# Performance work log

Hardware: AMD Instinct MI355X
Metric: run time of the kernel (lower is better)

## Reference

```python
import jax, jax.numpy as jnp
import numpy as np
import math

BS, N = 32, 2048
INPUT_SIZE, HIDDEN, NUM_LAYERS = 128, 64, 4
ALPHA, LAMDA = 0.1, 1.0
EPS = 1e-5
EDGE_P = 0.01


def setup_inputs() -> dict:
    key = jax.random.key(0)
    ks = jax.random.split(key, 6)
    x = jax.random.normal(ks[0], (BS, N, INPUT_SIZE), jnp.float32)
    adj = (jax.random.uniform(ks[1], (BS, N, N)) < EDGE_P).astype(jnp.float32)
    adj = adj * (1.0 - jnp.eye(N, dtype=jnp.float32))  # no pre-existing self loops
    proj_w = jax.random.normal(ks[2], (INPUT_SIZE, HIDDEN), jnp.float32) * (1.0 / math.sqrt(INPUT_SIZE))
    proj_b = jnp.zeros((HIDDEN,), jnp.float32)
    ln_g = jnp.ones((NUM_LAYERS, HIDDEN), jnp.float32)
    ln_b = jnp.zeros((NUM_LAYERS, HIDDEN), jnp.float32)
    conv_w = jax.random.normal(ks[3], (NUM_LAYERS, HIDDEN, HIDDEN), jnp.float32) * (1.0 / math.sqrt(HIDDEN))
    head_w = jax.random.normal(ks[4], (HIDDEN, 1), jnp.float32) * (1.0 / math.sqrt(HIDDEN))
    head_b = jnp.zeros((1,), jnp.float32)
    return dict(x=x, adj=adj, proj_w=proj_w, proj_b=proj_b, ln_g=ln_g, ln_b=ln_b,
                conv_w=conv_w, head_w=head_w, head_b=head_b)


def _layer_norm(h, g, b):
    mu = h.mean(-1, keepdims=True)
    var = ((h - mu) ** 2).mean(-1, keepdims=True)
    return (h - mu) * jax.lax.rsqrt(var + EPS) * g + b


def _gcn_norm(adj):
    # A_hat = D^{-1/2} (A + I) D^{-1/2}; only the nonzero pattern of adj is used,
    # matching adj.nonzero() -> edge_index with unit edge weights + added self loops.
    a = (adj != 0).astype(adj.dtype) + jnp.eye(adj.shape[-1], dtype=adj.dtype)
    dinv = jax.lax.rsqrt(a.sum(-1))  # deg >= 1 thanks to self loops
    return a * dinv[:, :, None] * dinv[:, None, :]


def _forward(x, adj_hat, proj_w, proj_b, ln_g, ln_b, conv_w, head_w, head_b):
    h = x @ proj_w + proj_b  # [bs, N, hidden]
    for i in range(NUM_LAYERS):
        beta = math.log(LAMDA / (i + 1) + 1.0)  # GCNII identity-mapping strength
        # DeepGCNLayer block='res+': h_in -> norm -> act -> conv, then residual add
        z = jax.nn.relu(_layer_norm(h, ln_g[i], ln_b[i]))
        p = jnp.einsum('bij,bjd->bid', adj_hat, z)          # neighbor aggregation
        s = (1.0 - ALPHA) * p + ALPHA * z                   # initial residual (x0 = conv input)
        h = h + (1.0 - beta) * s + beta * (s @ conv_w[i])   # GCN2Conv out + res+ skip
    return h @ head_w + head_b  # [bs, N, 1]


def reference(x, adj, proj_w, proj_b, ln_g, ln_b, conv_w, head_w, head_b):
    return _forward(x, _gcn_norm(adj), proj_w, proj_b, ln_g, ln_b, conv_w, head_w, head_b)
```

## Files before the change

### kernel.cpp

```cpp
#include <hip/hip_runtime.h>
#include <math.h>

#define BS 32
#define N 2048
#define ROWS (BS * N)
#define IN 128
#define HID 64
#define K_CAP 80
#define EPS 1e-5f
#define ALPHA 0.1f

typedef float fx4 __attribute__((ext_vector_type(4)));

__global__ __launch_bounds__(256) void k_build(const float* __restrict__ adj,
                                               int* __restrict__ ell,
                                               int* __restrict__ cnt,
                                               float* __restrict__ dinv) {
    int lane = threadIdx.x & 63;
    int row  = blockIdx.x * 4 + (threadIdx.x >> 6);
    const fx4* arow = (const fx4*)(adj + (size_t)row * N);
    int* erow = ell + (size_t)row * K_CAP;
    int base = 0;
#pragma unroll
    for (int it = 0; it < N / 256; it++) {
        fx4 f = __builtin_nontemporal_load(&arow[it * 64 + lane]);
#pragma unroll
        for (int k = 0; k < 4; k++) {
            float v = f[k];
            unsigned long long m = __ballot(v != 0.0f);
            if (v != 0.0f) {
                int pos = base + __popcll(m & ((1ull << lane) - 1ull));
                if (pos < K_CAP) erow[pos] = it * 256 + lane * 4 + k;
            }
            base += __popcll(m);
        }
    }
    if (lane == 0) {
        cnt[row]  = base < K_CAP ? base : K_CAP;
        dinv[row] = rsqrtf((float)base + 1.0f);
    }
}

__global__ __launch_bounds__(256) void k_proj_ln(const float* __restrict__ x,
                                                 const float* __restrict__ w,
                                                 const float* __restrict__ b,
                                                 const float* __restrict__ g0,
                                                 const float* __restrict__ b0,
                                                 float* __restrict__ h,
                                                 float* __restrict__ z0) {
    __shared__ float sw[IN * HID];
    __shared__ float sx[4][IN];
    int tx = threadIdx.x;
    for (int i = tx; i < IN * HID; i += 256) sw[i] = w[i];
    int row0 = blockIdx.x * 4;
    if (tx < 128) {
        float4 v = *(const float4*)(x + (size_t)(row0 + (tx >> 5)) * IN + (tx & 31) * 4);
        *(float4*)&sx[tx >> 5][(tx & 31) * 4] = v;
    }
    __syncthreads();
    int c = tx & 63, r = tx >> 6;
    float acc = b[c];
#pragma unroll
    for (int k = 0; k < IN; k += 4) {
        float4 xa = *(const float4*)&sx[r][k];
        acc += xa.x * sw[(k + 0) * HID + c];
        acc += xa.y * sw[(k + 1) * HID + c];
        acc += xa.z * sw[(k + 2) * HID + c];
        acc += xa.w * sw[(k + 3) * HID + c];
    }
    size_t idx = (size_t)(row0 + r) * HID + c;
    h[idx] = acc;
    float sum = acc;
    for (int o = 32; o >= 1; o >>= 1) sum += __shfl_xor(sum, o);
    float mu = sum * (1.0f / 64.0f);
    float d  = acc - mu;
    float vs = d * d;
    for (int o = 32; o >= 1; o >>= 1) vs += __shfl_xor(vs, o);
    float rr = rsqrtf(vs * (1.0f / 64.0f) + EPS);
    float zz = d * rr * g0[c] + b0[c];
    z0[idx] = zz > 0.0f ? zz : 0.0f;
}

__global__ __launch_bounds__(256) void k_layer(
    float* __restrict__ h, const float* __restrict__ z_in,
    float* __restrict__ z_out,
    const int* __restrict__ ell, const int* __restrict__ cnt,
    const float* __restrict__ dinv, const float* __restrict__ w,
    const float* __restrict__ g_next, const float* __restrict__ b_next,
    float beta, int is_last,
    const float* __restrict__ head_w, const float* __restrict__ head_b,
    float* __restrict__ out) {
    __shared__ float sw[HID * HID];
    __shared__ float ss[16][HID];
    int tx = threadIdx.x;
    int lane = tx & 63, wid = tx >> 6;
    int p = lane & 15, q = lane >> 4;

    int bid = blockIdx.x;
    int swz = (bid & 7) * (int)(gridDim.x >> 3) + (bid >> 3);
    int row0 = swz * 16 + wid * 4;
    int jbase = row0 & ~(N - 1);

    for (int i = tx; i < HID * HID; i += 256) sw[i] = w[i];

    int   nn[4];
    float di[4];
    int   myidx[4];
    float myw[4];
    float4 zi4[4];
#pragma unroll
    for (int rr = 0; rr < 4; rr++) {
        int row = row0 + rr;
        nn[rr] = cnt[row];
        di[rr] = dinv[row];
        zi4[rr] = *(const float4*)(z_in + (size_t)row * HID + 4 * p);
        myidx[rr] = 0; myw[rr] = 0.0f;
        if (lane < nn[rr]) {
            myidx[rr] = ell[(size_t)row * K_CAP + lane];
            myw[rr]   = dinv[jbase + myidx[rr]];
        }
    }

    float4 acc[4];
#pragma unroll
    for (int rr = 0; rr < 4; rr++) acc[rr] = make_float4(0.f, 0.f, 0.f, 0.f);
    int ntm = 0;
#pragma unroll
    for (int rr = 0; rr < 4; rr++) {
        int nm = nn[rr] < 64 ? nn[rr] : 64;
        nm = (nm + 3) & ~3;
        ntm = nm > ntm ? nm : ntm;
    }
    for (int t = q; t < ntm; t += 4) {
#pragma unroll
        for (int rr = 0; rr < 4; rr++) {
            int   j  = jbase + __shfl(myidx[rr], t);
            float wj = __shfl(myw[rr], t);
            float4 zj = *(const float4*)(z_in + (size_t)j * HID + 4 * p);
            acc[rr].x += wj * zj.x; acc[rr].y += wj * zj.y;
            acc[rr].z += wj * zj.z; acc[rr].w += wj * zj.w;
        }
    }
#pragma unroll
    for (int rr = 0; rr < 4; rr++) {
        for (int t = 64 + q; t < nn[rr]; t += 4) {
            int   j  = jbase + ell[(size_t)(row0 + rr) * K_CAP + t];
            float wj = dinv[j];
            float4 zj = *(const float4*)(z_in + (size_t)j * HID + 4 * p);
            acc[rr].x += wj * zj.x; acc[rr].y += wj * zj.y;
            acc[rr].z += wj * zj.z; acc[rr].w += wj * zj.w;
        }
    }
#pragma unroll
    for (int rr = 0; rr < 4; rr++) {
        float4 a = acc[rr];
        a.x += __shfl_xor(a.x, 16); a.y += __shfl_xor(a.y, 16);
        a.z += __shfl_xor(a.z, 16); a.w += __shfl_xor(a.w, 16);
        a.x += __shfl_xor(a.x, 32); a.y += __shfl_xor(a.y, 32);
        a.z += __shfl_xor(a.z, 32); a.w += __shfl_xor(a.w, 32);
        float dd = di[rr];
        float4 s4;
        s4.x = (1.0f - ALPHA) * dd * (a.x + dd * zi4[rr].x) + ALPHA * zi4[rr].x;
        s4.y = (1.0f - ALPHA) * dd * (a.y + dd * zi4[rr].y) + ALPHA * zi4[rr].y;
        s4.z = (1.0f - ALPHA) * dd * (a.z + dd * zi4[rr].z) + ALPHA * zi4[rr].z;
        s4.w = (1.0f - ALPHA) * dd * (a.w + dd * zi4[rr].w) + ALPHA * zi4[rr].w;
        if (q == 0) *(float4*)&ss[wid * 4 + rr][4 * p] = s4;
    }
    __syncthreads();

#pragma unroll
    for (int rr = 0; rr < 4; rr++) {
        int row = row0 + rr;
        float mv = 0.0f;
#pragma unroll
        for (int k = 0; k < HID; k += 4) {
            float4 sk = *(const float4*)&ss[wid * 4 + rr][k];
            mv += sk.x * sw[(k + 0) * HID + lane];
            mv += sk.y * sw[(k + 1) * HID + lane];
            mv += sk.z * sw[(k + 2) * HID + lane];
            mv += sk.w * sw[(k + 3) * HID + lane];
        }
        float s_c = ss[wid * 4 + rr][lane];
        size_t idx = (size_t)row * HID + lane;
        float hn = __builtin_nontemporal_load(h + idx) +
                   (1.0f - beta) * s_c + beta * mv;
        if (!is_last) {
            __builtin_nontemporal_store(hn, h + idx);
            float sum = hn;
            for (int o = 32; o >= 1; o >>= 1) sum += __shfl_xor(sum, o);
            float mu = sum * (1.0f / 64.0f);
            float d  = hn - mu;
            float vs = d * d;
            for (int o = 32; o >= 1; o >>= 1) vs += __shfl_xor(vs, o);
            float rv = rsqrtf(vs * (1.0f / 64.0f) + EPS);
            float zz = d * rv * g_next[lane] + b_next[lane];
            z_out[idx] = zz > 0.0f ? zz : 0.0f;
        } else {
            float v = hn * head_w[lane];
            for (int o = 32; o >= 1; o >>= 1) v += __shfl_xor(v, o);
            if (lane == 0) out[row] = v + head_b[0];
        }
    }
}

extern "C" void kernel_launch(void* const* d_in, const int* in_sizes, int n_in,
                              void* d_out, int out_size, void* d_ws, size_t ws_size,
                              hipStream_t stream) {
    const float* x      = (const float*)d_in[0];
    const float* adj    = (const float*)d_in[1];
    const float* proj_w = (const float*)d_in[2];
    const float* proj_b = (const float*)d_in[3];
    const float* ln_g   = (const float*)d_in[4];
    const float* ln_b   = (const float*)d_in[5];
    const float* conv_w = (const float*)d_in[6];
    const float* head_w = (const float*)d_in[7];
    const float* head_b = (const float*)d_in[8];
    float* out = (float*)d_out;

    float* h    = (float*)d_ws;
    float* za   = h + (size_t)ROWS * HID;
    float* zb   = za + (size_t)ROWS * HID;
    float* dinv = zb + (size_t)ROWS * HID;
    int*   cnt  = (int*)(dinv + ROWS);
    int*   ell  = cnt + ROWS;

    dim3 blk(256);

    k_build<<<dim3(ROWS / 4), blk, 0, stream>>>(adj, ell, cnt, dinv);
    k_proj_ln<<<dim3(ROWS / 4), blk, 0, stream>>>(x, proj_w, proj_b, ln_g, ln_b, h, za);

    float* zin = za;
    float* zout = zb;
    for (int i = 0; i < 4; i++) {
        float beta = (float)log(1.0 / (double)(i + 1) + 1.0);
        int last = (i == 3);
        int gi = (i + 1) < 3 ? (i + 1) : 3;
        k_layer<<<dim3(ROWS / 16), blk, 0, stream>>>(h, zin, zout, ell, cnt, dinv,
                                                     conv_w + (size_t)i * HID * HID,
                                                     ln_g + gi * HID, ln_b + gi * HID,
                                                     beta, last, head_w, head_b, out);
        float* t = zin; zin = zout; zout = t;
    }
}
```

Before: 407.0 us.

## Drop shared weight tile in layer kernel, read weights from global, raise occupancy

Removes the 16KB shared-memory copy of the conv weight and the block-wide barrier. The matvec now reads the weight directly from global/L1 and reuses each loaded weight across the wave's four rows. Also sets launch bounds to 8 waves per SIMD, defers the self-row z/dinv loads to lower register pressure, and uses 32-bit unsigned indexing with a precomputed batch base pointer. The intent is to cut LDS usage and register pressure so more blocks can be resident, which helps hide the latency of the gather. The cost is more global/L1 weight traffic and a risk of spilling under the tighter register bound. Dropping the barrier appears safe because each wave reads back only the ss rows it wrote itself.

```diff
diff --git a/kernel.cpp b/kernel.cpp
--- a/kernel.cpp
+++ b/kernel.cpp
@@ -81,7 +81,7 @@
     z0[idx] = zz > 0.0f ? zz : 0.0f;
 }
 
-__global__ __launch_bounds__(256) void k_layer(
+__global__ __launch_bounds__(256, 8) void k_layer(
     float* __restrict__ h, const float* __restrict__ z_in,
     float* __restrict__ z_out,
     const int* __restrict__ ell, const int* __restrict__ cnt,
@@ -90,7 +90,6 @@
     float beta, int is_last,
     const float* __restrict__ head_w, const float* __restrict__ head_b,
     float* __restrict__ out) {
-    __shared__ float sw[HID * HID];
     __shared__ float ss[16][HID];
     int tx = threadIdx.x;
     int lane = tx & 63, wid = tx >> 6;
@@ -100,30 +99,22 @@
     int swz = (bid & 7) * (int)(gridDim.x >> 3) + (bid >> 3);
     int row0 = swz * 16 + wid * 4;
     int jbase = row0 & ~(N - 1);
-
-    for (int i = tx; i < HID * HID; i += 256) sw[i] = w[i];
+    const float4* zb4 = (const float4*)z_in + (unsigned)jbase * 16u;
+    const float4* zr4 = (const float4*)z_in;
 
     int   nn[4];
-    float di[4];
     int   myidx[4];
     float myw[4];
-    float4 zi4[4];
 #pragma unroll
     for (int rr = 0; rr < 4; rr++) {
         int row = row0 + rr;
         nn[rr] = cnt[row];
-        di[rr] = dinv[row];
-        zi4[rr] = *(const float4*)(z_in + (size_t)row * HID + 4 * p);
         myidx[rr] = 0; myw[rr] = 0.0f;
         if (lane < nn[rr]) {
-            myidx[rr] = ell[(size_t)row * K_CAP + lane];
+            myidx[rr] = ell[(unsigned)row * K_CAP + lane];
             myw[rr]   = dinv[jbase + myidx[rr]];
         }
     }
-
-    float4 acc[4];
-#pragma unroll
-    for (int rr = 0; rr < 4; rr++) acc[rr] = make_float4(0.f, 0.f, 0.f, 0.f);
     int ntm = 0;
 #pragma unroll
     for (int rr = 0; rr < 4; rr++) {
@@ -131,12 +122,16 @@
         nm = (nm + 3) & ~3;
         ntm = nm > ntm ? nm : ntm;
     }
+
+    float4 acc[4];
+#pragma unroll
+    for (int rr = 0; rr < 4; rr++) acc[rr] = make_float4(0.f, 0.f, 0.f, 0.f);
     for (int t = q; t < ntm; t += 4) {
 #pragma unroll
         for (int rr = 0; rr < 4; rr++) {
-            int   j  = jbase + __shfl(myidx[rr], t);
+            int   j  = __shfl(myidx[rr], t);
             float wj = __shfl(myw[rr], t);
-            float4 zj = *(const float4*)(z_in + (size_t)j * HID + 4 * p);
+            float4 zj = zb4[(unsigned)(j * 16 + p)];
             acc[rr].x += wj * zj.x; acc[rr].y += wj * zj.y;
             acc[rr].z += wj * zj.z; acc[rr].w += wj * zj.w;
         }
@@ -144,13 +139,15 @@
 #pragma unroll
     for (int rr = 0; rr < 4; rr++) {
         for (int t = 64 + q; t < nn[rr]; t += 4) {
-            int   j  = jbase + ell[(size_t)(row0 + rr) * K_CAP + t];
+            int   j  = jbase + ell[(unsigned)(row0 + rr) * K_CAP + t];
             float wj = dinv[j];
-            float4 zj = *(const float4*)(z_in + (size_t)j * HID + 4 * p);
+            float4 zj = zr4[(unsigned)(j * 16 + p)];
             acc[rr].x += wj * zj.x; acc[rr].y += wj * zj.y;
             acc[rr].z += wj * zj.z; acc[rr].w += wj * zj.w;
         }
     }
+
+    const float c1 = 1.0f - ALPHA;
 #pragma unroll
     for (int rr = 0; rr < 4; rr++) {
         float4 a = acc[rr];
@@ -158,32 +155,38 @@
         a.z += __shfl_xor(a.z, 16); a.w += __shfl_xor(a.w, 16);
         a.x += __shfl_xor(a.x, 32); a.y += __shfl_xor(a.y, 32);
         a.z += __shfl_xor(a.z, 32); a.w += __shfl_xor(a.w, 32);
-        float dd = di[rr];
+        int row = row0 + rr;
+        float dd = dinv[row];
+        float4 zi = zr4[(unsigned)(row * 16 + p)];
         float4 s4;
-        s4.x = (1.0f - ALPHA) * dd * (a.x + dd * zi4[rr].x) + ALPHA * zi4[rr].x;
-        s4.y = (1.0f - ALPHA) * dd * (a.y + dd * zi4[rr].y) + ALPHA * zi4[rr].y;
-        s4.z = (1.0f - ALPHA) * dd * (a.z + dd * zi4[rr].z) + ALPHA * zi4[rr].z;
-        s4.w = (1.0f - ALPHA) * dd * (a.w + dd * zi4[rr].w) + ALPHA * zi4[rr].w;
+        s4.x = c1 * dd * (a.x + dd * zi.x) + ALPHA * zi.x;
+        s4.y = c1 * dd * (a.y + dd * zi.y) + ALPHA * zi.y;
+        s4.z = c1 * dd * (a.z + dd * zi.z) + ALPHA * zi.z;
+        s4.w = c1 * dd * (a.w + dd * zi.w) + ALPHA * zi.w;
         if (q == 0) *(float4*)&ss[wid * 4 + rr][4 * p] = s4;
     }
-    __syncthreads();
+
+    float mv[4] = {0.f, 0.f, 0.f, 0.f};
+#pragma unroll 4
+    for (int k = 0; k < HID; k += 4) {
+        float w0 = w[(unsigned)((k + 0) * HID + lane)];
+        float w1 = w[(unsigned)((k + 1) * HID + lane)];
+        float w2 = w[(unsigned)((k + 2) * HID + lane)];
+        float w3 = w[(unsigned)((k + 3) * HID + lane)];
+#pragma unroll
+        for (int rr = 0; rr < 4; rr++) {
+            float4 sk = *(const float4*)&ss[wid * 4 + rr][k];
+            mv[rr] += sk.x * w0 + sk.y * w1 + sk.z * w2 + sk.w * w3;
+        }
+    }
 
 #pragma unroll
     for (int rr = 0; rr < 4; rr++) {
         int row = row0 + rr;
-        float mv = 0.0f;
-#pragma unroll
-        for (int k = 0; k < HID; k += 4) {
-            float4 sk = *(const float4*)&ss[wid * 4 + rr][k];
-            mv += sk.x * sw[(k + 0) * HID + lane];
-            mv += sk.y * sw[(k + 1) * HID + lane];
-            mv += sk.z * sw[(k + 2) * HID + lane];
-            mv += sk.w * sw[(k + 3) * HID + lane];
-        }
         float s_c = ss[wid * 4 + rr][lane];
-        size_t idx = (size_t)row * HID + lane;
+        unsigned idx = (unsigned)(row * HID + lane);
         float hn = __builtin_nontemporal_load(h + idx) +
-                   (1.0f - beta) * s_c + beta * mv;
+                   (1.0f - beta) * s_c + beta * mv[rr];
         if (!is_last) {
             __builtin_nontemporal_store(hn, h + idx);
             float sum = hn;
```

Measured after the change: 398.6 us. 1.02x faster.
